# Kernel tuning notes

Measured on AMD Instinct MI355X. Metric: run time of the kernel, lower is better.

The kernel has to match this reference:

```python
import jax, jax.numpy as jnp
import numpy as np

B, IN, H, NC = 8192, 1024, 1024, 16
CS = H // NC  # chunk_size = 64


def cumsoftmax(x):
    # cumulative softmax along last dim
    return jnp.cumsum(jax.nn.softmax(x, axis=-1), axis=-1)


def setup_inputs() -> dict:
    key = jax.random.key(0)
    ks = jax.random.split(key, 9)
    s_ih = 1.0 / np.sqrt(IN)
    s_hh = 1.0 / np.sqrt(H)
    return {
        "x": jax.random.normal(ks[0], (B, IN), jnp.float32),
        "hx": jax.random.normal(ks[1], (B, H), jnp.float32),
        "cx": jax.random.normal(ks[2], (B, NC, CS), jnp.float32),
        "input_floor": jax.random.normal(ks[3], (B, NC), jnp.float32),
        "forget_floor": jax.random.normal(ks[4], (B, NC), jnp.float32),
        "W_ih": jax.random.uniform(ks[5], (4 * H, IN), jnp.float32, -s_ih, s_ih),
        "b_ih": jax.random.uniform(ks[6], (4 * H,), jnp.float32, -s_ih, s_ih),
        "W_hh": jax.random.uniform(ks[7], (4 * H, H), jnp.float32, -s_hh, s_hh),
        "b_hh": jax.random.uniform(ks[8], (4 * H,), jnp.float32, -s_hh, s_hh),
    }


def reference(x, hx, cx, input_floor, forget_floor, W_ih, b_ih, W_hh, b_hh):
    # dual GEMM (eval path: dropconnect=0.0 -> plain linear)
    gates = x @ W_ih.T + b_ih + hx @ W_hh.T + b_hh          # [B, 4H]
    g = gates.reshape(-1, NC * 4, CS)                        # [B, 4*NC, CS]
    outgate, cell, ingate, forgetgate = jnp.split(g, 4, axis=1)  # each [B, NC, CS]

    happy_in, sad_in = jnp.split(input_floor, 2, axis=1)     # [B, NC/2] each
    happy_fg, sad_fg = jnp.split(forget_floor, 2, axis=1)

    happy_cingate = cumsoftmax(happy_in)
    happy_cforgetgate = jnp.flip(cumsoftmax(jnp.flip(happy_fg, 1)), 1)
    sad_cingate = jnp.flip(cumsoftmax(jnp.flip(sad_in, 1)), 1)
    sad_cforgetgate = cumsoftmax(sad_fg)

    cingate = jnp.concatenate([happy_cingate, sad_cingate], axis=1)[:, :, None]      # [B, NC, 1]
    cforgetgate = jnp.concatenate([happy_cforgetgate, sad_cforgetgate], axis=1)[:, :, None]

    ingate = jax.nn.sigmoid(ingate)
    forgetgate = jax.nn.sigmoid(forgetgate)
    cell = jnp.tanh(cell)
    outgate = jax.nn.sigmoid(outgate)

    overlap = cforgetgate * cingate
    forgetgate = forgetgate * overlap + (cforgetgate - overlap)
    ingate = ingate * overlap + (cingate - overlap)

    cy = forgetgate * cx + ingate * cell                     # [B, NC, CS]
    hy = outgate * jnp.tanh(cy)
    return hy.reshape(-1, H), cy
```

## Files before the change

kernel.cpp:

```cpp
#include <hip/hip_runtime.h>
#include <hip/hip_bf16.h>


#define B_ROWS 8192
#define IN_DIM 1024
#define H_DIM  1024
#define NCHUNK 16
#define K_TOT  2048

#define BM   256
#define BN   256
#define BK   64
#define NKT  (K_TOT / BK)
#define THREADS 512

#define A_PACK_BYTES ((size_t)B_ROWS * K_TOT * 2)
#define W_PACK_BYTES ((size_t)16 * 256 * K_TOT * 2)

typedef __attribute__((ext_vector_type(4))) float  f32x4;
typedef __bf16 bf16x8 __attribute__((ext_vector_type(8)));

__device__ __forceinline__ float sigmoidf_(float x) {
    return 1.0f / (1.0f + __expf(-x));
}
__device__ __forceinline__ float tanhf_(float x) {
    float e = __expf(-2.0f * fabsf(x));
    float t = (1.0f - e) / (1.0f + e);
    return copysignf(t, x);
}

__device__ __forceinline__ void gload16(const __bf16* gsrc, __bf16* lds_dst) {
    __builtin_amdgcn_global_load_lds(
        (const __attribute__((address_space(1))) unsigned int*)gsrc,
        (__attribute__((address_space(3))) unsigned int*)lds_dst, 16, 0, 0);
}

__device__ __forceinline__ bf16x8 cvt8(f32x4 v0, f32x4 v1) {
    bf16x8 o;
    o[0] = (__bf16)v0.x; o[1] = (__bf16)v0.y; o[2] = (__bf16)v0.z; o[3] = (__bf16)v0.w;
    o[4] = (__bf16)v1.x; o[5] = (__bf16)v1.y; o[6] = (__bf16)v1.z; o[7] = (__bf16)v1.w;
    return o;
}

__global__ __launch_bounds__(256)
void pack_AW(const float* __restrict__ x, const float* __restrict__ hx,
             const float* __restrict__ W_ih, const float* __restrict__ W_hh,
             __bf16* __restrict__ Abf, __bf16* __restrict__ Wp)
{
    const int bid = blockIdx.x;
    const int c8  = threadIdx.x << 3;
    if (bid < B_ROWS) {
        const float* src = (c8 < IN_DIM)
            ? (x  + (size_t)bid * IN_DIM + c8)
            : (hx + (size_t)bid * IN_DIM + (c8 - IN_DIM));
        f32x4 v0 = *reinterpret_cast<const f32x4*>(src);
        f32x4 v1 = *reinterpret_cast<const f32x4*>(src + 4);
        *reinterpret_cast<bf16x8*>(Abf + (size_t)bid * K_TOT + c8) = cvt8(v0, v1);
    } else {
        const int r  = bid - B_ROWS;
        const int bh = r >> 8;
        const int n  = r & 255;
        const int g  = (n >> 4) & 3;
        const int j  = (n >> 6) * 16 + (n & 15);
        const int wr = g * H_DIM + bh * 64 + j;
        const float* src = (c8 < IN_DIM)
            ? (W_ih + (size_t)wr * IN_DIM + c8)
            : (W_hh + (size_t)wr * IN_DIM + (c8 - IN_DIM));
        f32x4 v0 = *reinterpret_cast<const f32x4*>(src);
        f32x4 v1 = *reinterpret_cast<const f32x4*>(src + 4);
        *reinterpret_cast<bf16x8*>(Wp + (size_t)r * K_TOT + c8) = cvt8(v0, v1);
    }
}

__device__ __forceinline__ void stage_half(const __bf16* __restrict__ gbase, int kb,
                                           __bf16* lbase, int row0, int tid) {
    #pragma unroll
    for (int i = 0; i < 2; ++i) {
        int e   = i * 4096 + tid * 8;
        int row = row0 + (e >> 6);
        int kd  = e & 63;
        gload16(gbase + (size_t)row * K_TOT + kb + (kd ^ ((row & 7) << 3)), lbase + e);
    }
}

#define SWZ(r, k) ((r) * 64 + ((k) ^ (((r) & 7) << 3)))

#define LDB(Bs) { \
    _Pragma("unroll") \
    for (int fn = 0; fn < 4; ++fn) { \
        int br = wcol + fn * 16 + lr; \
        bfr[fn][0] = *reinterpret_cast<const bf16x8*>(&(Bs)[SWZ(br, lh * 8)]); \
        bfr[fn][1] = *reinterpret_cast<const bf16x8*>(&(Bs)[SWZ(br, 32 + lh * 8)]); \
    } }

#define LDA_TO(dst, As, q) { \
    int ar = wrow + (q) * 32 + lr; \
    dst[0][0] = *reinterpret_cast<const bf16x8*>(&(As)[SWZ(ar, lh * 8)]); \
    dst[0][1] = *reinterpret_cast<const bf16x8*>(&(As)[SWZ(ar, 32 + lh * 8)]); \
    dst[1][0] = *reinterpret_cast<const bf16x8*>(&(As)[SWZ(ar + 16, lh * 8)]); \
    dst[1][1] = *reinterpret_cast<const bf16x8*>(&(As)[SWZ(ar + 16, 32 + lh * 8)]); \
    }

#define BARRIER do { \
    asm volatile("" ::: "memory"); \
    __builtin_amdgcn_s_barrier(); \
    asm volatile("" ::: "memory"); \
} while (0)

#define MF_Q(q, a) { \
    __builtin_amdgcn_s_setprio(1); \
    _Pragma("unroll") \
    for (int ks = 0; ks < 2; ++ks) { \
        _Pragma("unroll") \
        for (int fn = 0; fn < 4; ++fn) { \
            acc[2*(q)][fn]   = __builtin_amdgcn_mfma_f32_16x16x32_bf16(a[0][ks], bfr[fn][ks], acc[2*(q)][fn],   0,0,0); \
            acc[2*(q)+1][fn] = __builtin_amdgcn_mfma_f32_16x16x32_bf16(a[1][ks], bfr[fn][ks], acc[2*(q)+1][fn], 0,0,0); \
        } \
    } \
    __builtin_amdgcn_s_setprio(0); \
}

#define TILE11(T, Ac, An, Bc) { \
    const int t_ = (T); \
     \
    LDB(Bc); \
    LDA_TO(afE, Ac, 0); \
    LDA_TO(afO, Ac, 1); \
    stage_half(Arow, ((t_ + 1) & 31) * BK, An,        0,   tid); \
    stage_half(Arow, ((t_ + 1) & 31) * BK, An + 8192, 128, tid); \
    MF_Q(0, afE); \
    BARRIER; \
     \
    LDA_TO(afE, Ac, 2); \
    stage_half(Wblk, ((t_ + 2) & 31) * BK, Bc,        0,   tid); \
    MF_Q(1, afO); \
     \
    LDA_TO(afO, Ac, 3); \
    stage_half(Wblk, ((t_ + 2) & 31) * BK, Bc + 8192, 128, tid); \
    MF_Q(2, afE); \
     \
    MF_Q(3, afO); \
    asm volatile("s_waitcnt lgkmcnt(0)" ::: "memory"); \
    asm volatile("s_waitcnt vmcnt(4)"   ::: "memory"); \
    BARRIER; \
}

__global__ __launch_bounds__(THREADS, 2)
void onlstm_gemm11(const __bf16* __restrict__ Abf, const __bf16* __restrict__ Wp,
                   const float* __restrict__ cx,
                   const float* __restrict__ input_floor,
                   const float* __restrict__ forget_floor,
                   const float* __restrict__ b_ih, const float* __restrict__ b_hh,
                   float* __restrict__ out)
{
    __shared__ __align__(16) __bf16 lds[65536];
    __shared__ float ci_s[BM], cf_s[BM], bias_s[BN];

    const int tid = threadIdx.x;
    const int n0  = blockIdx.x;
    const int bm  = (n0 & 7) * 4 + ((n0 >> 3) & 3);
    const int bh  = n0 >> 5;
    const int h0  = bh * 64;
    const int nc  = bh;

    if (tid < BM) {
        {
            int g = (tid >> 4) & 3;
            int j = (tid >> 6) * 16 + (tid & 15);
            int wrr = g * H_DIM + h0 + j;
            bias_s[tid] = b_ih[wrr] + b_hh[wrr];
        }
        int b = bm * BM + tid;
        const int off = (nc < 8) ? 0 : 8;
        const int ic  = (nc < 8) ? nc : (nc - 8);
        const float* pin = input_floor  + (size_t)b * NCHUNK + off;
        const float* pfg = forget_floor + (size_t)b * NCHUNK + off;
        float vi[8], vf[8];
        float mi = -1e30f, mf = -1e30f;
        #pragma unroll
        for (int t = 0; t < 8; ++t) {
            vi[t] = pin[t]; vf[t] = pfg[t];
            mi = fmaxf(mi, vi[t]); mf = fmaxf(mf, vf[t]);
        }
        float si = 0.f, sf = 0.f;
        #pragma unroll
        for (int t = 0; t < 8; ++t) {
            vi[t] = __expf(vi[t] - mi); vf[t] = __expf(vf[t] - mf);
            si += vi[t]; sf += vf[t];
        }
        float pi = 0.f, pf = 0.f;
        #pragma unroll
        for (int t = 0; t < 8; ++t) { if (t <= ic) { pi += vi[t]; pf += vf[t]; } }
        float suf_i = si - pi + vi[ic];
        float suf_f = sf - pf + vf[ic];
        float civ, cfv;
        if (nc < 8) { civ = pi / si;    cfv = suf_f / sf; }
        else        { civ = suf_i / si; cfv = pf / sf;    }
        ci_s[tid] = civ; cf_s[tid] = cfv;
    }

    const __bf16* Arow = Abf + (size_t)(bm * BM) * K_TOT;
    const __bf16* Wblk = Wp  + (size_t)bh * 256 * K_TOT;
    __bf16* const A0p = lds;
    __bf16* const A1p = lds + 16384;
    __bf16* const B0p = lds + 32768;
    __bf16* const B1p = lds + 49152;

    stage_half(Arow, 0,  A0p,        0,   tid);
    stage_half(Arow, 0,  A0p + 8192, 128, tid);
    stage_half(Wblk, 0,  B0p,        0,   tid);
    stage_half(Wblk, 0,  B0p + 8192, 128, tid);
    stage_half(Wblk, BK, B1p,        0,   tid);
    stage_half(Wblk, BK, B1p + 8192, 128, tid);
    asm volatile("s_waitcnt lgkmcnt(0)" ::: "memory");
    asm volatile("s_waitcnt vmcnt(4)"   ::: "memory");
    __builtin_amdgcn_s_barrier();
    asm volatile("" ::: "memory");

    f32x4  acc[8][4];
    #pragma unroll
    for (int i = 0; i < 8; ++i)
        #pragma unroll
        for (int j = 0; j < 4; ++j) acc[i][j] = (f32x4){0.f, 0.f, 0.f, 0.f};
    bf16x8 afE[2][2], afO[2][2];
    bf16x8 bfr[4][2];

    const int l    = tid & 63;
    const int wid  = tid >> 6;
    const int wrw  = wid >> 2;
    const int wc   = wid & 3;
    const int lr   = l & 15;
    const int lh   = l >> 4;
    const int wrow = wrw * 128;
    const int wcol = wc * 64;

    #pragma unroll 1
    for (int it = 0; it < NKT / 2; ++it) {
        const int t = 2 * it;
        TILE11(t,     A0p, A1p, B0p);
        TILE11(t + 1, A1p, A0p, B1p);
    }
    asm volatile("s_waitcnt vmcnt(0) lgkmcnt(0)" ::: "memory");

    const size_t CY_OFF = (size_t)B_ROWS * H_DIM;
    const int hcol = h0 + wc * 16 + lr;
    #pragma unroll
    for (int m = 0; m < 8; ++m) {
        #pragma unroll
        for (int r = 0; r < 4; ++r) {
            int rt = wrow + m * 16 + lh * 4 + r;
            int b  = bm * BM + rt;
            float civ = ci_s[rt], cfv = cf_s[rt];
            float ovl = cfv * civ;
            float og = acc[m][0][r] + bias_s[wcol + lr];
            float cg = acc[m][1][r] + bias_s[wcol + 16 + lr];
            float ig = acc[m][2][r] + bias_s[wcol + 32 + lr];
            float fg = acc[m][3][r] + bias_s[wcol + 48 + lr];
            float i_s = sigmoidf_(ig);
            float f_s = sigmoidf_(fg);
            float c_t = tanhf_(cg);
            float o_s = sigmoidf_(og);
            float fq = f_s * ovl + (cfv - ovl);
            float iq = i_s * ovl + (civ - ovl);
            float cxv = cx[(size_t)b * H_DIM + hcol];
            float cyv = fq * cxv + iq * c_t;
            float hyv = o_s * tanhf_(cyv);
            out[(size_t)b * H_DIM + hcol] = hyv;
            out[CY_OFF + (size_t)b * H_DIM + hcol] = cyv;
        }
    }
}

extern "C" void kernel_launch(void* const* d_in, const int* in_sizes, int n_in,
                              void* d_out, int out_size, void* d_ws, size_t ws_size,
                              hipStream_t stream) {
    const float* x            = (const float*)d_in[0];
    const float* hx           = (const float*)d_in[1];
    const float* cx           = (const float*)d_in[2];
    const float* input_floor  = (const float*)d_in[3];
    const float* forget_floor = (const float*)d_in[4];
    const float* W_ih         = (const float*)d_in[5];
    const float* b_ih         = (const float*)d_in[6];
    const float* W_hh         = (const float*)d_in[7];
    const float* b_hh         = (const float*)d_in[8];
    float* out = (float*)d_out;

    __bf16* Abf = (__bf16*)d_ws;
    __bf16* Wp  = (__bf16*)((char*)d_ws + A_PACK_BYTES);
    pack_AW<<<B_ROWS + 16 * 256, 256, 0, stream>>>(x, hx, W_ih, W_hh, Abf, Wp);
    onlstm_gemm11<<<512, THREADS, 0, stream>>>(
        Abf, Wp, cx, input_floor, forget_floor, b_ih, b_hh, out);
}
```

Measured before the change: 154.2 us.

## Use 16 waves per block with 64x64 warp tiles in the fused GEMM

Doubles the threads per block from 512 to 1024 and halves each wave's output tile from 128x64 to 64x64. Accumulator and A-fragment registers shrink accordingly, and global-to-LDS staging now issues one load per thread instead of two, with the vmcnt waits adjusted to match. The goal is more waves per SIMD to hide latency. The trade-off is that each B fragment read from LDS now feeds half as many MFMAs, which raises LDS traffic per flop. The launch bound of 4 blocks may also force tight register limits.

```diff
diff --git a/kernel.cpp b/kernel.cpp
--- a/kernel.cpp
+++ b/kernel.cpp
@@ -12,7 +12,7 @@
 #define BN   256
 #define BK   64
 #define NKT  (K_TOT / BK)
-#define THREADS 512
+#define THREADS 1024
 
 #define A_PACK_BYTES ((size_t)B_ROWS * K_TOT * 2)
 #define W_PACK_BYTES ((size_t)16 * 256 * K_TOT * 2)
@@ -74,13 +74,10 @@
 
 __device__ __forceinline__ void stage_half(const __bf16* __restrict__ gbase, int kb,
                                            __bf16* lbase, int row0, int tid) {
-    #pragma unroll
-    for (int i = 0; i < 2; ++i) {
-        int e   = i * 4096 + tid * 8;
-        int row = row0 + (e >> 6);
-        int kd  = e & 63;
-        gload16(gbase + (size_t)row * K_TOT + kb + (kd ^ ((row & 7) << 3)), lbase + e);
-    }
+    int e   = tid * 8;
+    int row = row0 + (e >> 6);
+    int kd  = e & 63;
+    gload16(gbase + (size_t)row * K_TOT + kb + (kd ^ ((row & 7) << 3)), lbase + e);
 }
 
 #define SWZ(r, k) ((r) * 64 + ((k) ^ (((r) & 7) << 3)))
@@ -93,12 +90,10 @@
         bfr[fn][1] = *reinterpret_cast<const bf16x8*>(&(Bs)[SWZ(br, 32 + lh * 8)]); \
     } }
 
-#define LDA_TO(dst, As, q) { \
-    int ar = wrow + (q) * 32 + lr; \
-    dst[0][0] = *reinterpret_cast<const bf16x8*>(&(As)[SWZ(ar, lh * 8)]); \
-    dst[0][1] = *reinterpret_cast<const bf16x8*>(&(As)[SWZ(ar, 32 + lh * 8)]); \
-    dst[1][0] = *reinterpret_cast<const bf16x8*>(&(As)[SWZ(ar + 16, lh * 8)]); \
-    dst[1][1] = *reinterpret_cast<const bf16x8*>(&(As)[SWZ(ar + 16, 32 + lh * 8)]); \
+#define LDA(As, q) { \
+    int ar = wrow + (q) * 16 + lr; \
+    af[0] = *reinterpret_cast<const bf16x8*>(&(As)[SWZ(ar, lh * 8)]); \
+    af[1] = *reinterpret_cast<const bf16x8*>(&(As)[SWZ(ar, 32 + lh * 8)]); \
     }
 
 #define BARRIER do { \
@@ -107,46 +102,45 @@
     asm volatile("" ::: "memory"); \
 } while (0)
 
-#define MF_Q(q, a) { \
+#define MF_Q(q) { \
     __builtin_amdgcn_s_setprio(1); \
     _Pragma("unroll") \
     for (int ks = 0; ks < 2; ++ks) { \
         _Pragma("unroll") \
         for (int fn = 0; fn < 4; ++fn) { \
-            acc[2*(q)][fn]   = __builtin_amdgcn_mfma_f32_16x16x32_bf16(a[0][ks], bfr[fn][ks], acc[2*(q)][fn],   0,0,0); \
-            acc[2*(q)+1][fn] = __builtin_amdgcn_mfma_f32_16x16x32_bf16(a[1][ks], bfr[fn][ks], acc[2*(q)+1][fn], 0,0,0); \
+            acc[q][fn] = __builtin_amdgcn_mfma_f32_16x16x32_bf16(af[ks], bfr[fn][ks], acc[q][fn], 0, 0, 0); \
         } \
     } \
     __builtin_amdgcn_s_setprio(0); \
 }
 
-#define TILE11(T, Ac, An, Bc) { \
+#define TILE12(T, Ac, An, Bc) { \
     const int t_ = (T); \
      \
     LDB(Bc); \
-    LDA_TO(afE, Ac, 0); \
-    LDA_TO(afO, Ac, 1); \
+    LDA(Ac, 0); \
     stage_half(Arow, ((t_ + 1) & 31) * BK, An,        0,   tid); \
     stage_half(Arow, ((t_ + 1) & 31) * BK, An + 8192, 128, tid); \
-    MF_Q(0, afE); \
+    MF_Q(0); \
     BARRIER; \
      \
-    LDA_TO(afE, Ac, 2); \
+    LDA(Ac, 1); \
     stage_half(Wblk, ((t_ + 2) & 31) * BK, Bc,        0,   tid); \
-    MF_Q(1, afO); \
-     \
-    LDA_TO(afO, Ac, 3); \
+    MF_Q(1); \
+     \
+    LDA(Ac, 2); \
     stage_half(Wblk, ((t_ + 2) & 31) * BK, Bc + 8192, 128, tid); \
-    MF_Q(2, afE); \
-     \
-    MF_Q(3, afO); \
+    MF_Q(2); \
+     \
+    LDA(Ac, 3); \
+    MF_Q(3); \
     asm volatile("s_waitcnt lgkmcnt(0)" ::: "memory"); \
-    asm volatile("s_waitcnt vmcnt(4)"   ::: "memory"); \
+    asm volatile("s_waitcnt vmcnt(2)"   ::: "memory"); \
     BARRIER; \
 }
 
-__global__ __launch_bounds__(THREADS, 2)
-void onlstm_gemm11(const __bf16* __restrict__ Abf, const __bf16* __restrict__ Wp,
+__global__ __launch_bounds__(THREADS, 4)
+void onlstm_gemm12(const __bf16* __restrict__ Abf, const __bf16* __restrict__ Wp,
                    const float* __restrict__ cx,
                    const float* __restrict__ input_floor,
                    const float* __restrict__ forget_floor,
@@ -213,16 +207,16 @@
     stage_half(Wblk, BK, B1p,        0,   tid);
     stage_half(Wblk, BK, B1p + 8192, 128, tid);
     asm volatile("s_waitcnt lgkmcnt(0)" ::: "memory");
-    asm volatile("s_waitcnt vmcnt(4)"   ::: "memory");
+    asm volatile("s_waitcnt vmcnt(2)"   ::: "memory");
     __builtin_amdgcn_s_barrier();
     asm volatile("" ::: "memory");
 
-    f32x4  acc[8][4];
+    f32x4  acc[4][4];
     #pragma unroll
-    for (int i = 0; i < 8; ++i)
+    for (int i = 0; i < 4; ++i)
         #pragma unroll
         for (int j = 0; j < 4; ++j) acc[i][j] = (f32x4){0.f, 0.f, 0.f, 0.f};
-    bf16x8 afE[2][2], afO[2][2];
+    bf16x8 af[2];
     bf16x8 bfr[4][2];
 
     const int l    = tid & 63;
@@ -231,21 +225,21 @@
     const int wc   = wid & 3;
     const int lr   = l & 15;
     const int lh   = l >> 4;
-    const int wrow = wrw * 128;
+    const int wrow = wrw * 64;
     const int wcol = wc * 64;
 
     #pragma unroll 1
     for (int it = 0; it < NKT / 2; ++it) {
         const int t = 2 * it;
-        TILE11(t,     A0p, A1p, B0p);
-        TILE11(t + 1, A1p, A0p, B1p);
+        TILE12(t,     A0p, A1p, B0p);
+        TILE12(t + 1, A1p, A0p, B1p);
     }
     asm volatile("s_waitcnt vmcnt(0) lgkmcnt(0)" ::: "memory");
 
     const size_t CY_OFF = (size_t)B_ROWS * H_DIM;
     const int hcol = h0 + wc * 16 + lr;
     #pragma unroll
-    for (int m = 0; m < 8; ++m) {
+    for (int m = 0; m < 4; ++m) {
         #pragma unroll
         for (int r = 0; r < 4; ++r) {
             int rt = wrow + m * 16 + lh * 4 + r;
@@ -288,6 +282,6 @@
     __bf16* Abf = (__bf16*)d_ws;
     __bf16* Wp  = (__bf16*)((char*)d_ws + A_PACK_BYTES);
     pack_AW<<<B_ROWS + 16 * 256, 256, 0, stream>>>(x, hx, W_ih, W_hh, Abf, Wp);
-    onlstm_gemm11<<<512, THREADS, 0, stream>>>(
+    onlstm_gemm12<<<512, THREADS, 0, stream>>>(
         Abf, Wp, cx, input_floor, forget_floor, b_ih, b_hh, out);
 }
```

Result: slower. 161.3 us (+4.7%).

## Split MFMA tile loop by k-half to shrink fragment registers and prefetch across tiles

Applied to the files above, without the earlier changes.

Restructures the GEMM inner tile so LDS fragment loads and MFMAs run over the two 32-wide k halves in turn. A and B fragments shrink to single k-slices, and the first A fragment of the next tile is loaded before the loop-ending barrier completes its use. This aims to cut register pressure and to interleave LDS reads with MFMAs more finely, hiding LDS latency. In exchange it adds an extra lgkmcnt wait in mid-tile and moves the barrier. The cross-tile prefetch also reads the next buffer right after the barrier, which relies on the vmcnt accounting staying correct.

```diff
diff --git a/kernel.cpp b/kernel.cpp
--- a/kernel.cpp
+++ b/kernel.cpp
@@ -85,20 +85,17 @@
 
 #define SWZ(r, k) ((r) * 64 + ((k) ^ (((r) & 7) << 3)))
 
-#define LDB(Bs) { \
+#define LDB_KS(dst, Bs, ks) { \
     _Pragma("unroll") \
     for (int fn = 0; fn < 4; ++fn) { \
         int br = wcol + fn * 16 + lr; \
-        bfr[fn][0] = *reinterpret_cast<const bf16x8*>(&(Bs)[SWZ(br, lh * 8)]); \
-        bfr[fn][1] = *reinterpret_cast<const bf16x8*>(&(Bs)[SWZ(br, 32 + lh * 8)]); \
+        dst[fn] = *reinterpret_cast<const bf16x8*>(&(Bs)[SWZ(br, (ks) * 32 + lh * 8)]); \
     } }
 
-#define LDA_TO(dst, As, q) { \
+#define LDA_QK(dst, As, q, ks) { \
     int ar = wrow + (q) * 32 + lr; \
-    dst[0][0] = *reinterpret_cast<const bf16x8*>(&(As)[SWZ(ar, lh * 8)]); \
-    dst[0][1] = *reinterpret_cast<const bf16x8*>(&(As)[SWZ(ar, 32 + lh * 8)]); \
-    dst[1][0] = *reinterpret_cast<const bf16x8*>(&(As)[SWZ(ar + 16, lh * 8)]); \
-    dst[1][1] = *reinterpret_cast<const bf16x8*>(&(As)[SWZ(ar + 16, 32 + lh * 8)]); \
+    dst[0] = *reinterpret_cast<const bf16x8*>(&(As)[SWZ(ar,      (ks) * 32 + lh * 8)]); \
+    dst[1] = *reinterpret_cast<const bf16x8*>(&(As)[SWZ(ar + 16, (ks) * 32 + lh * 8)]); \
     }
 
 #define BARRIER do { \
@@ -106,47 +103,58 @@
     __builtin_amdgcn_s_barrier(); \
     asm volatile("" ::: "memory"); \
 } while (0)
-
-#define MF_Q(q, a) { \
+#define LGKM0 asm volatile("s_waitcnt lgkmcnt(0)" ::: "memory")
+
+#define MF8(q, a, b) { \
     __builtin_amdgcn_s_setprio(1); \
     _Pragma("unroll") \
-    for (int ks = 0; ks < 2; ++ks) { \
-        _Pragma("unroll") \
-        for (int fn = 0; fn < 4; ++fn) { \
-            acc[2*(q)][fn]   = __builtin_amdgcn_mfma_f32_16x16x32_bf16(a[0][ks], bfr[fn][ks], acc[2*(q)][fn],   0,0,0); \
-            acc[2*(q)+1][fn] = __builtin_amdgcn_mfma_f32_16x16x32_bf16(a[1][ks], bfr[fn][ks], acc[2*(q)+1][fn], 0,0,0); \
-        } \
+    for (int fn = 0; fn < 4; ++fn) { \
+        acc[2*(q)][fn]   = __builtin_amdgcn_mfma_f32_16x16x32_bf16(a[0], b[fn], acc[2*(q)][fn],   0, 0, 0); \
+        acc[2*(q)+1][fn] = __builtin_amdgcn_mfma_f32_16x16x32_bf16(a[1], b[fn], acc[2*(q)+1][fn], 0, 0, 0); \
     } \
     __builtin_amdgcn_s_setprio(0); \
 }
 
-#define TILE11(T, Ac, An, Bc) { \
+#define TILE14(T, Ac, An, Bc) { \
     const int t_ = (T); \
      \
-    LDB(Bc); \
-    LDA_TO(afE, Ac, 0); \
-    LDA_TO(afO, Ac, 1); \
+    LDB_KS(bf0, Bc, 0); \
+    LDA_QK(afO, Ac, 1, 0); \
     stage_half(Arow, ((t_ + 1) & 31) * BK, An,        0,   tid); \
+    MF8(0, afE, bf0); \
+     \
+    LDA_QK(afE, Ac, 2, 0); \
     stage_half(Arow, ((t_ + 1) & 31) * BK, An + 8192, 128, tid); \
-    MF_Q(0, afE); \
+    MF8(1, afO, bf0); \
+     \
+    LDA_QK(afO, Ac, 3, 0); \
+    MF8(2, afE, bf0); \
+     \
+    LDB_KS(bf1, Bc, 1); \
+    LDA_QK(afE, Ac, 0, 1); \
+    MF8(3, afO, bf0); \
+    LGKM0; BARRIER; \
+     \
+    LDA_QK(afO, Ac, 1, 1); \
+    stage_half(Wblk, ((t_ + 2) & 31) * BK, Bc,        0,   tid); \
+    MF8(0, afE, bf1); \
+     \
+    LDA_QK(afE, Ac, 2, 1); \
+    stage_half(Wblk, ((t_ + 2) & 31) * BK, Bc + 8192, 128, tid); \
+    MF8(1, afO, bf1); \
+     \
+    LDA_QK(afO, Ac, 3, 1); \
+    MF8(2, afE, bf1); \
+     \
+    MF8(3, afO, bf1); \
+    LGKM0; \
+    asm volatile("s_waitcnt vmcnt(4)" ::: "memory"); \
     BARRIER; \
-     \
-    LDA_TO(afE, Ac, 2); \
-    stage_half(Wblk, ((t_ + 2) & 31) * BK, Bc,        0,   tid); \
-    MF_Q(1, afO); \
-     \
-    LDA_TO(afO, Ac, 3); \
-    stage_half(Wblk, ((t_ + 2) & 31) * BK, Bc + 8192, 128, tid); \
-    MF_Q(2, afE); \
-     \
-    MF_Q(3, afO); \
-    asm volatile("s_waitcnt lgkmcnt(0)" ::: "memory"); \
-    asm volatile("s_waitcnt vmcnt(4)"   ::: "memory"); \
-    BARRIER; \
+    LDA_QK(afE, An, 0, 0);    \
 }
 
 __global__ __launch_bounds__(THREADS, 2)
-void onlstm_gemm11(const __bf16* __restrict__ Abf, const __bf16* __restrict__ Wp,
+void onlstm_gemm14(const __bf16* __restrict__ Abf, const __bf16* __restrict__ Wp,
                    const float* __restrict__ cx,
                    const float* __restrict__ input_floor,
                    const float* __restrict__ forget_floor,
@@ -212,8 +220,8 @@
     stage_half(Wblk, 0,  B0p + 8192, 128, tid);
     stage_half(Wblk, BK, B1p,        0,   tid);
     stage_half(Wblk, BK, B1p + 8192, 128, tid);
-    asm volatile("s_waitcnt lgkmcnt(0)" ::: "memory");
-    asm volatile("s_waitcnt vmcnt(4)"   ::: "memory");
+    LGKM0;
+    asm volatile("s_waitcnt vmcnt(4)" ::: "memory");
     __builtin_amdgcn_s_barrier();
     asm volatile("" ::: "memory");
 
@@ -222,8 +230,8 @@
     for (int i = 0; i < 8; ++i)
         #pragma unroll
         for (int j = 0; j < 4; ++j) acc[i][j] = (f32x4){0.f, 0.f, 0.f, 0.f};
-    bf16x8 afE[2][2], afO[2][2];
-    bf16x8 bfr[4][2];
+    bf16x8 afE[2], afO[2];
+    bf16x8 bf0[4], bf1[4];
 
     const int l    = tid & 63;
     const int wid  = tid >> 6;
@@ -234,11 +242,13 @@
     const int wrow = wrw * 128;
     const int wcol = wc * 64;
 
+    LDA_QK(afE, A0p, 0, 0);
+
     #pragma unroll 1
     for (int it = 0; it < NKT / 2; ++it) {
         const int t = 2 * it;
-        TILE11(t,     A0p, A1p, B0p);
-        TILE11(t + 1, A1p, A0p, B1p);
+        TILE14(t,     A0p, A1p, B0p);
+        TILE14(t + 1, A1p, A0p, B1p);
     }
     asm volatile("s_waitcnt vmcnt(0) lgkmcnt(0)" ::: "memory");
 
@@ -288,6 +298,6 @@
     __bf16* Abf = (__bf16*)d_ws;
     __bf16* Wp  = (__bf16*)((char*)d_ws + A_PACK_BYTES);
     pack_AW<<<B_ROWS + 16 * 256, 256, 0, stream>>>(x, hx, W_ih, W_hh, Abf, Wp);
-    onlstm_gemm11<<<512, THREADS, 0, stream>>>(
+    onlstm_gemm14<<<512, THREADS, 0, stream>>>(
         Abf, Wp, cx, input_floor, forget_floor, b_ih, b_hh, out);
 }
```

After: 165.9 us. +7.6%, slower.

## Fuse activation fp32-to-bf16 conversion into GEMM main loop

Applied to the files above, without the earlier changes.

Drops the separate pass that converted x and hx to a packed bf16 buffer. The GEMM now loads fp32 activation tiles into registers a stage ahead, converts them, and writes them into swizzled LDS between MFMA groups. This removes a full write and re-read of the 32 MB bf16 activation buffer, but each activation tile is now read as fp32 by every one of the 16 column blocks. It also adds register pressure and synchronous VGPR-to-LDS stores in place of direct global-to-LDS loads.

```diff
diff --git a/kernel.cpp b/kernel.cpp
--- a/kernel.cpp
+++ b/kernel.cpp
@@ -14,10 +14,8 @@
 #define NKT  (K_TOT / BK)
 #define THREADS 512
 
-#define A_PACK_BYTES ((size_t)B_ROWS * K_TOT * 2)
-#define W_PACK_BYTES ((size_t)16 * 256 * K_TOT * 2)
-
 typedef __attribute__((ext_vector_type(4))) float  f32x4;
+typedef __bf16 bf16x4 __attribute__((ext_vector_type(4)));
 typedef __bf16 bf16x8 __attribute__((ext_vector_type(8)));
 
 __device__ __forceinline__ float sigmoidf_(float x) {
@@ -43,33 +41,22 @@
 }
 
 __global__ __launch_bounds__(256)
-void pack_AW(const float* __restrict__ x, const float* __restrict__ hx,
-             const float* __restrict__ W_ih, const float* __restrict__ W_hh,
-             __bf16* __restrict__ Abf, __bf16* __restrict__ Wp)
+void pack_W(const float* __restrict__ W_ih, const float* __restrict__ W_hh,
+            __bf16* __restrict__ Wp)
 {
-    const int bid = blockIdx.x;
-    const int c8  = threadIdx.x << 3;
-    if (bid < B_ROWS) {
-        const float* src = (c8 < IN_DIM)
-            ? (x  + (size_t)bid * IN_DIM + c8)
-            : (hx + (size_t)bid * IN_DIM + (c8 - IN_DIM));
-        f32x4 v0 = *reinterpret_cast<const f32x4*>(src);
-        f32x4 v1 = *reinterpret_cast<const f32x4*>(src + 4);
-        *reinterpret_cast<bf16x8*>(Abf + (size_t)bid * K_TOT + c8) = cvt8(v0, v1);
-    } else {
-        const int r  = bid - B_ROWS;
-        const int bh = r >> 8;
-        const int n  = r & 255;
-        const int g  = (n >> 4) & 3;
-        const int j  = (n >> 6) * 16 + (n & 15);
-        const int wr = g * H_DIM + bh * 64 + j;
-        const float* src = (c8 < IN_DIM)
-            ? (W_ih + (size_t)wr * IN_DIM + c8)
-            : (W_hh + (size_t)wr * IN_DIM + (c8 - IN_DIM));
-        f32x4 v0 = *reinterpret_cast<const f32x4*>(src);
-        f32x4 v1 = *reinterpret_cast<const f32x4*>(src + 4);
-        *reinterpret_cast<bf16x8*>(Wp + (size_t)r * K_TOT + c8) = cvt8(v0, v1);
-    }
+    const int r  = blockIdx.x;
+    const int c8 = threadIdx.x << 3;
+    const int bh = r >> 8;
+    const int n  = r & 255;
+    const int g  = (n >> 4) & 3;
+    const int j  = (n >> 6) * 16 + (n & 15);
+    const int wr = g * H_DIM + bh * 64 + j;
+    const float* src = (c8 < IN_DIM)
+        ? (W_ih + (size_t)wr * IN_DIM + c8)
+        : (W_hh + (size_t)wr * IN_DIM + (c8 - IN_DIM));
+    f32x4 v0 = *reinterpret_cast<const f32x4*>(src);
+    f32x4 v1 = *reinterpret_cast<const f32x4*>(src + 4);
+    *reinterpret_cast<bf16x8*>(Wp + (size_t)r * K_TOT + c8) = cvt8(v0, v1);
 }
 
 __device__ __forceinline__ void stage_half(const __bf16* __restrict__ gbase, int kb,
@@ -101,11 +88,33 @@
     dst[1][1] = *reinterpret_cast<const bf16x8*>(&(As)[SWZ(ar + 16, 32 + lh * 8)]); \
     }
 
+#define ALOAD(T1) { \
+    const int tt_ = (T1) & 31; \
+    const float* As_ = (tt_ < 16) ? (xg + tt_ * BK) : (hxg + (tt_ * BK - IN_DIM)); \
+    _Pragma("unroll") \
+    for (int j = 0; j < 8; ++j) { \
+        int e = j * 2048 + tid * 4; \
+        av[j] = *reinterpret_cast<const f32x4*>( \
+            As_ + (size_t)(bm * BM + (e >> 6)) * IN_DIM + (e & 63)); \
+    } }
+
+#define AWRITE(An, j0) { \
+    _Pragma("unroll") \
+    for (int j = (j0); j < (j0) + 4; ++j) { \
+        int e = j * 2048 + tid * 4; \
+        int row = e >> 6; int kd = e & 63; \
+        bf16x4 s4; \
+        s4[0] = (__bf16)av[j].x; s4[1] = (__bf16)av[j].y; \
+        s4[2] = (__bf16)av[j].z; s4[3] = (__bf16)av[j].w; \
+        *reinterpret_cast<bf16x4*>(&(An)[SWZ(row, kd)]) = s4; \
+    } }
+
 #define BARRIER do { \
     asm volatile("" ::: "memory"); \
     __builtin_amdgcn_s_barrier(); \
     asm volatile("" ::: "memory"); \
 } while (0)
+#define LGKM0 asm volatile("s_waitcnt lgkmcnt(0)" ::: "memory")
 
 #define MF_Q(q, a) { \
     __builtin_amdgcn_s_setprio(1); \
@@ -120,14 +129,13 @@
     __builtin_amdgcn_s_setprio(0); \
 }
 
-#define TILE11(T, Ac, An, Bc) { \
+#define TILE15(T, Ac, An, Bc) { \
     const int t_ = (T); \
      \
     LDB(Bc); \
     LDA_TO(afE, Ac, 0); \
     LDA_TO(afO, Ac, 1); \
-    stage_half(Arow, ((t_ + 1) & 31) * BK, An,        0,   tid); \
-    stage_half(Arow, ((t_ + 1) & 31) * BK, An + 8192, 128, tid); \
+    ALOAD(t_ + 1); \
     MF_Q(0, afE); \
     BARRIER; \
      \
@@ -137,16 +145,18 @@
      \
     LDA_TO(afO, Ac, 3); \
     stage_half(Wblk, ((t_ + 2) & 31) * BK, Bc + 8192, 128, tid); \
+    AWRITE(An, 0); \
     MF_Q(2, afE); \
      \
+    AWRITE(An, 4); \
     MF_Q(3, afO); \
-    asm volatile("s_waitcnt lgkmcnt(0)" ::: "memory"); \
-    asm volatile("s_waitcnt vmcnt(4)"   ::: "memory"); \
+    LGKM0; \
     BARRIER; \
 }
 
 __global__ __launch_bounds__(THREADS, 2)
-void onlstm_gemm11(const __bf16* __restrict__ Abf, const __bf16* __restrict__ Wp,
+void onlstm_gemm15(const float* __restrict__ xg, const float* __restrict__ hxg,
+                   const __bf16* __restrict__ Wp,
                    const float* __restrict__ cx,
                    const float* __restrict__ input_floor,
                    const float* __restrict__ forget_floor,
@@ -199,31 +209,11 @@
         ci_s[tid] = civ; cf_s[tid] = cfv;
     }
 
-    const __bf16* Arow = Abf + (size_t)(bm * BM) * K_TOT;
-    const __bf16* Wblk = Wp  + (size_t)bh * 256 * K_TOT;
+    const __bf16* Wblk = Wp + (size_t)bh * 256 * K_TOT;
     __bf16* const A0p = lds;
     __bf16* const A1p = lds + 16384;
     __bf16* const B0p = lds + 32768;
     __bf16* const B1p = lds + 49152;
-
-    stage_half(Arow, 0,  A0p,        0,   tid);
-    stage_half(Arow, 0,  A0p + 8192, 128, tid);
-    stage_half(Wblk, 0,  B0p,        0,   tid);
-    stage_half(Wblk, 0,  B0p + 8192, 128, tid);
-    stage_half(Wblk, BK, B1p,        0,   tid);
-    stage_half(Wblk, BK, B1p + 8192, 128, tid);
-    asm volatile("s_waitcnt lgkmcnt(0)" ::: "memory");
-    asm volatile("s_waitcnt vmcnt(4)"   ::: "memory");
-    __builtin_amdgcn_s_barrier();
-    asm volatile("" ::: "memory");
-
-    f32x4  acc[8][4];
-    #pragma unroll
-    for (int i = 0; i < 8; ++i)
-        #pragma unroll
-        for (int j = 0; j < 4; ++j) acc[i][j] = (f32x4){0.f, 0.f, 0.f, 0.f};
-    bf16x8 afE[2][2], afO[2][2];
-    bf16x8 bfr[4][2];
 
     const int l    = tid & 63;
     const int wid  = tid >> 6;
@@ -234,11 +224,33 @@
     const int wrow = wrw * 128;
     const int wcol = wc * 64;
 
+    f32x4 av[8];
+
+    stage_half(Wblk, 0,  B0p,        0,   tid);
+    stage_half(Wblk, 0,  B0p + 8192, 128, tid);
+    stage_half(Wblk, BK, B1p,        0,   tid);
+    stage_half(Wblk, BK, B1p + 8192, 128, tid);
+    ALOAD(0);
+    AWRITE(A0p, 0);
+    AWRITE(A0p, 4);
+    LGKM0;
+    asm volatile("s_waitcnt vmcnt(4)" ::: "memory");
+    __builtin_amdgcn_s_barrier();
+    asm volatile("" ::: "memory");
+
+    f32x4  acc[8][4];
+    #pragma unroll
+    for (int i = 0; i < 8; ++i)
+        #pragma unroll
+        for (int j = 0; j < 4; ++j) acc[i][j] = (f32x4){0.f, 0.f, 0.f, 0.f};
+    bf16x8 afE[2][2], afO[2][2];
+    bf16x8 bfr[4][2];
+
     #pragma unroll 1
     for (int it = 0; it < NKT / 2; ++it) {
         const int t = 2 * it;
-        TILE11(t,     A0p, A1p, B0p);
-        TILE11(t + 1, A1p, A0p, B1p);
+        TILE15(t,     A0p, A1p, B0p);
+        TILE15(t + 1, A1p, A0p, B1p);
     }
     asm volatile("s_waitcnt vmcnt(0) lgkmcnt(0)" ::: "memory");
 
@@ -285,9 +297,8 @@
     const float* b_hh         = (const float*)d_in[8];
     float* out = (float*)d_out;
 
-    __bf16* Abf = (__bf16*)d_ws;
-    __bf16* Wp  = (__bf16*)((char*)d_ws + A_PACK_BYTES);
-    pack_AW<<<B_ROWS + 16 * 256, 256, 0, stream>>>(x, hx, W_ih, W_hh, Abf, Wp);
-    onlstm_gemm11<<<512, THREADS, 0, stream>>>(
-        Abf, Wp, cx, input_floor, forget_floor, b_ih, b_hh, out);
-}
+    __bf16* Wp = (__bf16*)d_ws;
+    pack_W<<<16 * 256, 256, 0, stream>>>(W_ih, W_hh, Wp);
+    onlstm_gemm15<<<512, THREADS, 0, stream>>>(
+        x, hx, Wp, cx, input_floor, forget_floor, b_ih, b_hh, out);
+}
```

After: 341.9 us. 122% more time.
